# Kernel optimization log

Measured on AMD Instinct MI355X. Metric: run time of the kernel, lower is better.

Reference implementation:

```python
import jax, jax.numpy as jnp
import numpy as np


def setup_inputs() -> dict:
    key = jax.random.key(0)
    x = jax.random.normal(key, (16, 256, 256, 64), dtype=jnp.float32)
    return {"x": x, "n_components": 32}


def reference(x, n_components):
    B = x.shape[0]
    C = x.shape[-1]
    # flatten spatial dims: [B, N, C]
    flat = x.reshape(B, -1, C)
    N = flat.shape[1]
    mean = jnp.mean(flat, axis=1, keepdims=True)
    centered = flat - mean
    # per-batch covariance [B, C, C]
    cov = jnp.einsum('bnc,bnd->bcd', centered, centered) / jnp.float32(N - 1)
    eigenvalues, eigenvectors = jnp.linalg.eigh(cov)
    # sort eigenvectors by descending eigenvalue, keep top n_components columns
    idx = jnp.argsort(-eigenvalues, axis=-1)  # [B, C]
    top = jnp.take_along_axis(eigenvectors, idx[:, None, :], axis=-1)[:, :, :n_components]
    # project: [B, N, k]
    projected = jnp.einsum('bnc,bck->bnk', centered, top)
    return projected.reshape(x.shape[:-1] + (n_components,))
```

## Files before the change

### kernel.cpp

```cpp
#include <hip/hip_runtime.h>
#include <hip/hip_bf16.h>


__device__ __forceinline__ double fsign(double a, double b){ return (b >= 0.0) ? fabs(a) : -fabs(a); }
__device__ __forceinline__ double slapy2(double x, double y){ return sqrt(x*x + y*y); }

__device__ __forceinline__ void slartg(double f, double g, double& cs, double& sn, double& r){
  if (g == 0.0){ cs = 1.0; sn = 0.0; r = f; }
  else if (f == 0.0){ cs = 0.0; sn = fsign(1.0, g); r = fabs(g); }
  else {
    double d = sqrt(f*f + g*g);
    cs = fabs(f)/d;
    r  = fsign(d, f);
    sn = g/r;
  }
}

__device__ __forceinline__ void slaev2(double a, double b, double c,
                                       double& rt1, double& rt2, double& cs1, double& sn1){
  double sm = a + c, df = a - c, adf = fabs(df), tb = b + b, ab = fabs(tb);
  double acmx, acmn, rt, cs, ct, acs, tn; int sgn1, sgn2;
  if (fabs(a) > fabs(c)) { acmx = a; acmn = c; } else { acmx = c; acmn = a; }
  if (adf > ab)      rt = adf*sqrt(1.0 + (ab/adf)*(ab/adf));
  else if (adf < ab) rt = ab*sqrt(1.0 + (adf/ab)*(adf/ab));
  else               rt = ab*sqrt(2.0);
  if (sm < 0.0){ rt1 = 0.5*(sm - rt); sgn1 = -1; rt2 = (acmx/rt1)*acmn - (b/rt1)*b; }
  else if (sm > 0.0){ rt1 = 0.5*(sm + rt); sgn1 = 1; rt2 = (acmx/rt1)*acmn - (b/rt1)*b; }
  else { rt1 = 0.5*rt; rt2 = -0.5*rt; sgn1 = 1; }
  if (df >= 0.0){ cs = df + rt; sgn2 = 1; } else { cs = df - rt; sgn2 = -1; }
  acs = fabs(cs);
  if (acs > ab){ ct = -tb/cs; sn1 = 1.0/sqrt(1.0 + ct*ct); cs1 = ct*sn1; }
  else {
    if (ab == 0.0){ cs1 = 1.0; sn1 = 0.0; }
    else { tn = -cs/tb; cs1 = 1.0/sqrt(1.0 + tn*tn); sn1 = tn*cs1; }
  }
  if (sgn1 == sgn2){ tn = cs1; cs1 = -sn1; sn1 = tn; }
}

__device__ __forceinline__ double wave_sum(double v){
  #pragma unroll
  for (int off = 32; off > 0; off >>= 1) v += __shfl_xor(v, off);
  return v;
}

template<int LDZ>
__device__ void steqr16(double* dd, double* ee, double* Zt, int tid,
                        double* wc, double* wsn)
{
#define DQ(i) dd[(i)-1]
#define EQ(i) ee[(i)-1]
#define ZT(r,c) Zt[(r)*LDZ+(c)]
  const int n = 16;
  const double eps = 5.9604644775390625e-8;
  const double eps2 = eps*eps;
  const double safmin = 1.1754943508222875e-38;
  const int nmaxit = n*30;
  int jtot = 0, l1 = 1, nm1 = n-1;
  int l, lsv, lend, lendsv, m, i;
  double p, g, r, s, c, f, b2, rt1, rt2, anorm, tst;

L10:
  if (l1 > n) goto L160;
  if (l1 > 1) EQ(l1-1) = 0.0;
  if (l1 <= nm1){
    for (m = l1; m <= nm1; ++m){
      tst = fabs(EQ(m));
      if (tst == 0.0) goto L30;
      if (tst <= (sqrt(fabs(DQ(m)))*sqrt(fabs(DQ(m+1))))*eps){ EQ(m) = 0.0; goto L30; }
    }
  }
  m = n;
L30:
  l = l1; lsv = l; lend = m; lendsv = lend; l1 = m+1;
  if (lend == l) goto L10;
  anorm = 0.0;
  for (i = l; i <= lend; ++i) anorm = fmax(anorm, fabs(DQ(i)));
  for (i = l; i <  lend; ++i) anorm = fmax(anorm, fabs(EQ(i)));
  if (anorm == 0.0) goto L10;
  if (fabs(DQ(lend)) < fabs(DQ(l))){ lend = lsv; l = lendsv; }
  if (lend > l){
L40:
    if (l != lend){
      for (m = l; m <= lend-1; ++m){
        tst = fabs(EQ(m)); tst = tst*tst;
        if (tst <= (eps2*fabs(DQ(m)))*fabs(DQ(m+1)) + safmin) goto L60;
      }
    }
    m = lend;
L60:
    if (m < lend) EQ(m) = 0.0;
    p = DQ(l);
    if (m == l) goto L80;
    if (m == l+1){
      slaev2(DQ(l), EQ(l), DQ(l+1), rt1, rt2, c, s);
      if (tid < 16){
        double t = ZT(tid, l);
        ZT(tid, l)   = c*t - s*ZT(tid, l-1);
        ZT(tid, l-1) = s*t + c*ZT(tid, l-1);
      }
      DQ(l) = rt1; DQ(l+1) = rt2; EQ(l) = 0.0;
      l += 2;
      if (l <= lend) goto L40;
      goto L140;
    }
    if (jtot == nmaxit) goto L140;
    jtot++;
    g = (DQ(l+1)-p)/(2.0*EQ(l));
    r = slapy2(g, 1.0);
    g = DQ(m) - p + (EQ(l)/(g + fsign(r, g)));
    s = 1.0; c = 1.0; p = 0.0;
    for (i = m-1; i >= l; --i){
      f = s*EQ(i); b2 = c*EQ(i);
      slartg(g, f, c, s, r);
      if (i != m-1) EQ(i+1) = r;
      g = DQ(i+1) - p;
      r = (DQ(i)-g)*s + 2.0*c*b2;
      p = s*r;
      DQ(i+1) = g + p;
      g = c*r - b2;
      wc[i] = c; wsn[i] = -s;
    }
    for (int i2 = m-1; i2 >= l; --i2){
      double cc = wc[i2], ssv = wsn[i2];
      if (tid < 16){
        double t = ZT(tid, i2);
        ZT(tid, i2)   = cc*t - ssv*ZT(tid, i2-1);
        ZT(tid, i2-1) = ssv*t + cc*ZT(tid, i2-1);
      }
    }
    DQ(l) = DQ(l) - p;
    EQ(l) = g;
    goto L40;
L80:
    DQ(l) = p;
    l++;
    if (l <= lend) goto L40;
    goto L140;
  } else {
L90:
    if (l != lend){
      for (m = l; m >= lend+1; --m){
        tst = fabs(EQ(m-1)); tst = tst*tst;
        if (tst <= (eps2*fabs(DQ(m)))*fabs(DQ(m-1)) + safmin) goto L110;
      }
    }
    m = lend;
L110:
    if (m > lend) EQ(m-1) = 0.0;
    p = DQ(l);
    if (m == l) goto L130;
    if (m == l-1){
      slaev2(DQ(l-1), EQ(l-1), DQ(l), rt1, rt2, c, s);
      if (tid < 16){
        double t = ZT(tid, l-1);
        ZT(tid, l-1) = c*t - s*ZT(tid, l-2);
        ZT(tid, l-2) = s*t + c*ZT(tid, l-2);
      }
      DQ(l-1) = rt1; DQ(l) = rt2; EQ(l-1) = 0.0;
      l -= 2;
      if (l >= lend) goto L90;
      goto L140;
    }
    if (jtot == nmaxit) goto L140;
    jtot++;
    g = (DQ(l-1)-p)/(2.0*EQ(l-1));
    r = slapy2(g, 1.0);
    g = DQ(m) - p + (EQ(l-1)/(g + fsign(r, g)));
    s = 1.0; c = 1.0; p = 0.0;
    for (i = m; i <= l-1; ++i){
      f = s*EQ(i); b2 = c*EQ(i);
      slartg(g, f, c, s, r);
      if (i != m) EQ(i-1) = r;
      g = DQ(i) - p;
      r = (DQ(i+1)-g)*s + 2.0*c*b2;
      p = s*r;
      DQ(i) = g + p;
      g = c*r - b2;
      wc[i] = c; wsn[i] = s;
    }
    for (int i2 = m; i2 <= l-1; ++i2){
      double cc = wc[i2], ssv = wsn[i2];
      if (tid < 16){
        double t = ZT(tid, i2);
        ZT(tid, i2)   = cc*t - ssv*ZT(tid, i2-1);
        ZT(tid, i2-1) = ssv*t + cc*ZT(tid, i2-1);
      }
    }
    DQ(l) = DQ(l) - p;
    EQ(l-1) = g;
    goto L90;
L130:
    DQ(l) = p;
    l--;
    if (l >= lend) goto L90;
    goto L140;
  }
L140:
  if (jtot < nmaxit) goto L10;
L160:
  for (int ii = 2; ii <= n; ++ii){
    int i3 = ii-1, k2 = i3;
    p = DQ(i3);
    for (int j = ii; j <= n; ++j) if (DQ(j) < p){ k2 = j; p = DQ(j); }
    if (k2 != i3){
      DQ(k2) = DQ(i3); DQ(i3) = p;
      if (tid < 16){
        double t = ZT(tid, i3-1);
        ZT(tid, i3-1) = ZT(tid, k2-1);
        ZT(tid, k2-1) = t;
      }
    }
  }
#undef DQ
#undef EQ
#undef ZT
}

template<int N1, int LD>
__device__ void merge_dc(double* Z, double* dloc, double rho_in, int tid,
                         double* zz, double* dl, double* ww, double* mu, double* wt,
                         int* idxm, int* sv, int* tl, int* fperm)
{
  const int NM = 2*N1;
  const int Q  = NM/4;
  const double eps32 = 5.9604644775390625e-8;
  const int j4 = tid >> 2, part = tid & 3;
  __shared__ int s_kn[2];

  if (tid < N1)       zz[tid] = Z[(N1-1)*LD + tid];
  else if (tid < NM)  zz[tid] = Z[N1*LD + tid];
  __syncthreads();
  if (rho_in < 0.0 && tid >= N1 && tid < NM) zz[tid] = -zz[tid];
  __syncthreads();
  if (tid < NM) zz[tid] *= 0.70710678118654752440;
  __syncthreads();
  double rho = fabs(2.0*rho_in);

  {
    int i1 = 0, i2 = 0, t = 0;
    while (i1 < N1 && i2 < N1){
      if (dloc[i1] <= dloc[N1+i2]) idxm[t++] = i1++;
      else                         idxm[t++] = N1 + (i2++);
    }
    while (i1 < N1) idxm[t++] = i1++;
    while (i2 < N1) idxm[t++] = N1 + (i2++);
  }
  double dmax = 0.0, zmax = 0.0;
  for (int i = 0; i < NM; ++i){ dmax = fmax(dmax, fabs(dloc[i])); zmax = fmax(zmax, fabs(zz[i])); }
  double tol = 8.0*eps32*fmax(dmax, zmax);

  if (rho*zmax <= tol){
    double colr[Q]; double dnj = 0.0;
    if (j4 < NM){
      int s0 = idxm[j4];
      dnj = dloc[s0];
      #pragma unroll
      for (int rr = 0; rr < Q; ++rr) colr[rr] = Z[(part+4*rr)*LD + s0];
    }
    __syncthreads();
    if (j4 < NM){
      #pragma unroll
      for (int rr = 0; rr < Q; ++rr) Z[(part+4*rr)*LD + j4] = colr[rr];
      if (part == 0) dloc[j4] = dnj;
    }
    __syncthreads();
    return;
  }

  int K, nd;
  if (tid < 64){
    K = 0; nd = 0;
    int have = 0, pj = 0;
    for (int t = 0; t < NM; ++t){
      int nj = idxm[t];
      if (rho*fabs(zz[nj]) <= tol){
        for (int q = nd; q > 0; --q) tl[q] = tl[q-1];
        tl[0] = nj; nd++;
        continue;
      }
      if (!have){ pj = nj; have = 1; continue; }
      {
        double sZ = zz[pj], cZ = zz[nj];
        double tau2 = slapy2(cZ, sZ);
        double tgap = dloc[nj] - dloc[pj];
        cZ /= tau2; sZ = -sZ/tau2;
        if (fabs(tgap*cZ*sZ) <= tol){
          zz[nj] = tau2; zz[pj] = 0.0;
          if (tid < NM){
            double xq = Z[tid*LD + pj], yq = Z[tid*LD + nj];
            Z[tid*LD + pj] = cZ*xq + sZ*yq;
            Z[tid*LD + nj] = cZ*yq - sZ*xq;
          }
          double t2 = dloc[pj]*cZ*cZ + dloc[nj]*sZ*sZ;
          double t3 = dloc[pj]*sZ*sZ + dloc[nj]*cZ*cZ;
          dloc[nj] = t3; dloc[pj] = t2;
          for (int q = nd; q > 0; --q) tl[q] = tl[q-1];
          tl[0] = pj; nd++;
          { int q = 0;
            while (q+1 < nd && dloc[tl[q]] < dloc[tl[q+1]]){
              int tt = tl[q]; tl[q] = tl[q+1]; tl[q+1] = tt; q++;
            } }
          pj = nj;
        } else {
          sv[K] = pj; dl[K] = dloc[pj]; ww[K] = zz[pj]; K++;
          pj = nj;
        }
      }
    }
    sv[K] = pj; dl[K] = dloc[pj]; ww[K] = zz[pj]; K++;
    if (tid == 0){ s_kn[0] = K; s_kn[1] = nd; }
  }
  __syncthreads();
  K = s_kn[0]; nd = s_kn[1];

  if (j4 < K){
    double dj = dl[j4];
    double dlr[Q], wr[Q];
    double zs2p = 0.0;
    #pragma unroll
    for (int t = 0; t < Q; ++t){
      int i = part + 4*t;
      if (i < K){ double wv = ww[i]; dlr[t] = dl[i]; wr[t] = rho*wv*wv; zs2p += wv*wv; }
      else      { dlr[t] = 1.0e300; wr[t] = 0.0; }
    }
    zs2p += __shfl_xor(zs2p, 1); zs2p += __shfl_xor(zs2p, 2);
    double lo = 0.0, hi = (j4 < K-1) ? (dl[j4+1]-dj) : rho*zs2p;
    for (int it = 0; it < 24; ++it){
      double mid = 0.5*(lo+hi);
      if (mid == lo || mid == hi) break;
      double fvp = 0.0;
      #pragma unroll
      for (int t = 0; t < Q; ++t) fvp += wr[t]/((dlr[t]-dj) - mid);
      fvp += __shfl_xor(fvp, 1); fvp += __shfl_xor(fvp, 2);
      double fv = 1.0 + fvp;
      if (fv < 0.0) lo = mid; else hi = mid;
    }
    double muv = 0.5*(lo+hi);
    for (int it = 0; it < 14; ++it){
      double fvp = 0.0, fpp = 0.0;
      #pragma unroll
      for (int t = 0; t < Q; ++t){
        double den = (dlr[t]-dj) - muv;
        double inv = 1.0/den;
        double tq = wr[t]*inv;
        fvp += tq; fpp += tq*inv;
      }
      fvp += __shfl_xor(fvp, 1); fvp += __shfl_xor(fvp, 2);
      fpp += __shfl_xor(fpp, 1); fpp += __shfl_xor(fpp, 2);
      double fv = 1.0 + fvp;
      if (fv == 0.0) break;
      if (fv < 0.0) lo = muv; else hi = muv;
      double mn = muv - fv/fpp;
      if (!(mn > lo && mn < hi)) mn = 0.5*(lo+hi);
      if (mn == muv) break;
      muv = mn;
    }
    if (part == 0) mu[j4] = muv;
  }
  __syncthreads();

  if (j4 < K){
    double dj = dl[j4];
    double pp = 1.0;
    for (int i2 = part; i2 < K; i2 += 4){
      if (i2 == j4) continue;
      double dij = dj - dl[i2];
      pp *= (dij - mu[i2])/dij;
    }
    pp *= __shfl_xor(pp, 1); pp *= __shfl_xor(pp, 2);
    double prod = -mu[j4]*pp;
    if (part == 0) wt[j4] = fsign(sqrt(fmax(-prod, 0.0)), ww[j4]);
  }
  __syncthreads();

  {
    int a = 0, q = nd-1, t = 0;
    while (a < K && q >= 0){
      if (dl[a]+mu[a] <= dloc[tl[q]]) { fperm[t++] = a; a++; }
      else { fperm[t++] = K+q; q--; }
    }
    while (a < K)  { fperm[t++] = a; a++; }
    while (q >= 0) { fperm[t++] = K+q; q--; }
  }
  __syncthreads();

  double colr[Q]; double dnj = 0.0;
  if (j4 < NM){
    int src = fperm[j4];
    if (src < K){
      double muj = mu[src];
      double ds  = dl[src];
      double nrmp = 0.0;
      for (int i = part; i < K; i += 4){
        double del = (dl[i]-ds) - muj;
        double qv = wt[i]/del;
        nrmp += qv*qv;
      }
      nrmp += __shfl_xor(nrmp, 1); nrmp += __shfl_xor(nrmp, 2);
      double invn = 1.0/sqrt(nrmp);
      #pragma unroll
      for (int rr = 0; rr < Q; ++rr) colr[rr] = 0.0;
      for (int i = 0; i < K; ++i){
        double del = (dl[i]-ds) - muj;
        double sval = (wt[i]/del)*invn;
        int cq = sv[i];
        #pragma unroll
        for (int rr = 0; rr < Q; ++rr) colr[rr] += Z[(part+4*rr)*LD + cq]*sval;
      }
      dnj = ds + muj;
    } else {
      int tq2 = tl[src-K];
      #pragma unroll
      for (int rr = 0; rr < Q; ++rr) colr[rr] = Z[(part+4*rr)*LD + tq2];
      dnj = dloc[tq2];
    }
  }
  __syncthreads();
  if (j4 < NM){
    #pragma unroll
    for (int rr = 0; rr < Q; ++rr) Z[(part+4*rr)*LD + j4] = colr[rr];
    if (part == 0) dloc[j4] = dnj;
  }
  __syncthreads();
}

__global__ __launch_bounds__(256) void cov_kernel(const float* __restrict__ x,
                                                  double* __restrict__ gram,
                                                  double* __restrict__ chsum)
{
  __shared__ __align__(16) float tile[16][64];
  const int b   = blockIdx.x >> 5;
  const int ch  = blockIdx.x & 31;
  const int tid = threadIdx.x;
  const int ti = tid >> 4, tj = tid & 15;
  const int lrow = tid >> 4, lf4 = tid & 15;
  const int cch = tid & 63, crr = tid >> 6;
  float acc[4][4];
  #pragma unroll
  for (int a = 0; a < 4; ++a)
    #pragma unroll
    for (int c = 0; c < 4; ++c) acc[a][c] = 0.f;
  float csum = 0.f;
  const int rbase = ch*2048;
  for (int r0 = 0; r0 < 2048; r0 += 16){
    const float4 v = *(const float4*)(x + (((size_t)b*65536 + rbase + r0 + lrow)*64 + lf4*4));
    __syncthreads();
    *(float4*)&tile[lrow][lf4*4] = v;
    __syncthreads();
    #pragma unroll
    for (int rr = 0; rr < 16; ++rr){
      float4 xi = *(const float4*)&tile[rr][4*ti];
      float4 xj = *(const float4*)&tile[rr][4*tj];
      acc[0][0] += xi.x*xj.x; acc[0][1] += xi.x*xj.y; acc[0][2] += xi.x*xj.z; acc[0][3] += xi.x*xj.w;
      acc[1][0] += xi.y*xj.x; acc[1][1] += xi.y*xj.y; acc[1][2] += xi.y*xj.z; acc[1][3] += xi.y*xj.w;
      acc[2][0] += xi.z*xj.x; acc[2][1] += xi.z*xj.y; acc[2][2] += xi.z*xj.z; acc[2][3] += xi.z*xj.w;
      acc[3][0] += xi.w*xj.x; acc[3][1] += xi.w*xj.y; acc[3][2] += xi.w*xj.z; acc[3][3] += xi.w*xj.w;
    }
    #pragma unroll
    for (int rr2 = 0; rr2 < 4; ++rr2) csum += tile[crr + rr2*4][cch];
  }
  double* gb = gram + (size_t)b*4096;
  #pragma unroll
  for (int a = 0; a < 4; ++a)
    #pragma unroll
    for (int c = 0; c < 4; ++c)
      atomicAdd(&gb[(4*ti+a)*64 + (4*tj+c)], (double)acc[a][c]);
  atomicAdd(&chsum[b*64 + cch], (double)csum);
}

__global__ __launch_bounds__(64) void tridiag_kernel(const double* __restrict__ gram,
                                                     const double* __restrict__ chsum,
                                                     double* __restrict__ dG,
                                                     double* __restrict__ eG,
                                                     double* __restrict__ tauG,
                                                     double* __restrict__ VlG,
                                                     float* __restrict__ meanG)
{
  __shared__ double As[64*65];
  __shared__ double vv_[64], wv_[64], mu_s[64], es_s[64], tau_s[64];
  const int b = blockIdx.x;
  const int tid = threadIdx.x;
  const double* gb = gram + (size_t)b*4096;

  double mval = chsum[b*64+tid]*(1.0/65536.0);
  meanG[b*64+tid] = (float)mval;
  mu_s[tid] = mval;
  __syncthreads();
  for (int idx = tid; idx < 4096; idx += 64){
    int i = idx >> 6, j = idx & 63;
    As[i*65+j] = (gb[idx] - 65536.0*mu_s[i]*mu_s[j])*(1.0/65535.0);
  }
  __syncthreads();

  for (int i = 0; i < 63; ++i){
    double alpha = As[(i+1)*65+i];
    double xv0 = (tid >= i+2) ? As[tid*65+i] : 0.0;
    double xn2 = wave_sum(xv0*xv0);
    if (xn2 == 0.0){
      es_s[i] = alpha; tau_s[i] = 0.0;
      VlG[((size_t)b*63 + i)*64 + tid] = 0.0;
      __syncthreads();
      continue;
    }
    double xnorm = sqrt(xn2);
    double betav = -fsign(slapy2(alpha, xnorm), alpha);
    double taui  = (betav-alpha)/betav;
    double invs  = 1.0/(alpha-betav);
    double vval = (tid == i+1) ? 1.0 : ((tid >= i+2) ? xv0*invs : 0.0);
    vv_[tid] = vval;
    VlG[((size_t)b*63 + i)*64 + tid] = vval;
    __syncthreads();
    double xvr = 0.0;
    if (tid >= i+1){
      for (int c2 = i+1; c2 < 64; ++c2) xvr += As[tid*65+c2]*vv_[c2];
      xvr *= taui;
    }
    double dot = wave_sum((tid >= i+1) ? xvr*vval : 0.0);
    double alf = -0.5*taui*dot;
    wv_[tid] = (tid >= i+1) ? (xvr + alf*vval) : 0.0;
    __syncthreads();
    if (tid >= i+1){
      double vr = vval, wr = wv_[tid];
      for (int c2 = i+1; c2 < 64; ++c2) As[tid*65+c2] -= vr*wv_[c2] + wr*vv_[c2];
    }
    es_s[i] = betav; tau_s[i] = taui;
    __syncthreads();
  }
  dG[b*64+tid]   = As[tid*65+tid];
  eG[b*64+tid]   = (tid < 63) ? es_s[tid]  : 0.0;
  tauG[b*64+tid] = (tid < 63) ? tau_s[tid] : 0.0;
}

__global__ __launch_bounds__(64) void steqr_kernel(double* __restrict__ dG,
                                                   const double* __restrict__ eG,
                                                   double* __restrict__ Zg)
{
  __shared__ double Zt[16*17];
  __shared__ double dd[16], ee[16], wc[20], wsn[20];
  const int b = blockIdx.x >> 2, s = blockIdx.x & 3;
  const int tid = threadIdx.x;

  {
    double dv = (tid < 16) ? dG[b*64 + 16*s + tid] : 0.0;
    if (tid == 0  && s > 0) dv -= fabs(eG[b*64 + 16*s - 1]);
    if (tid == 15 && s < 3) dv -= fabs(eG[b*64 + 16*s + 15]);
    if (tid < 16) dd[tid] = dv;
    if (tid < 15) ee[tid] = eG[b*64 + 16*s + tid];
    if (tid == 15) ee[15] = 0.0;
  }
  for (int idx = tid; idx < 16*17; idx += 64) Zt[idx] = 0.0;
  __syncthreads();
  if (tid < 16) Zt[tid*17+tid] = 1.0;
  __syncthreads();

  steqr16<17>(dd, ee, Zt, tid, wc, wsn);
  __syncthreads();

  for (int idx = tid; idx < 256; idx += 64){
    int r = idx >> 4, c = idx & 15;
    Zg[(size_t)b*4096 + s*256 + idx] = Zt[r*17+c];
  }
  if (tid < 16) dG[b*64 + 16*s + tid] = dd[tid];
}

__global__ __launch_bounds__(256) void merge16_kernel(double* __restrict__ Zg,
                                                      double* __restrict__ dG,
                                                      const double* __restrict__ eG)
{
  __shared__ double Z32[32*33];
  __shared__ double dloc[32];
  __shared__ double zz[32], dl[32], ww[32], mu[32], wt[32];
  __shared__ int idxm[32], sv[32], tl[32], fp[32];
  const int b = blockIdx.x >> 1, h = blockIdx.x & 1;
  const int tid = threadIdx.x;

  for (int idx = tid; idx < 32*33; idx += 256) Z32[idx] = 0.0;
  if (tid < 32) dloc[tid] = dG[b*64 + 32*h + tid];
  __syncthreads();
  {
    int idx = tid;
    int r = idx >> 4, c = idx & 15;
    Z32[r*33 + c]           = Zg[(size_t)b*4096 + (2*h)*256   + idx];
    Z32[(16+r)*33 + (16+c)] = Zg[(size_t)b*4096 + (2*h+1)*256 + idx];
  }
  __syncthreads();

  double rho_in = eG[b*64 + 32*h + 15];
  merge_dc<16,33>(Z32, dloc, rho_in, tid, zz, dl, ww, mu, wt, idxm, sv, tl, fp);

  for (int idx = tid; idx < 1024; idx += 256){
    int r = idx >> 5, c = idx & 31;
    Zg[(size_t)b*4096 + 2048 + h*1024 + idx] = Z32[r*33 + c];
  }
  if (tid < 32) dG[b*64 + 32*h + tid] = dloc[tid];
}

__global__ __launch_bounds__(256) void merge32_bt_kernel(const double* __restrict__ Zg,
                                                         double* __restrict__ dG,
                                                         const double* __restrict__ eG,
                                                         const double* __restrict__ tauG,
                                                         const double* __restrict__ VlG,
                                                         float* __restrict__ Vt)
{
  __shared__ double Z64[64*65];
  __shared__ double Vl_s[63*64];
  __shared__ double dloc[64], tau_l[64];
  __shared__ double zz[64], dl[64], ww[64], mu[64], wt[64];
  __shared__ int idxm[64], sv[64], tl[64], fp[64];
  const int b = blockIdx.x;
  const int tid = threadIdx.x;

  for (int idx = tid; idx < 64*65; idx += 256) Z64[idx] = 0.0;
  if (tid < 64){ dloc[tid] = dG[b*64 + tid]; tau_l[tid] = tauG[b*64 + tid]; }
  for (int idx = tid; idx < 63*64; idx += 256) Vl_s[idx] = VlG[(size_t)b*63*64 + idx];
  __syncthreads();
  for (int idx = tid; idx < 1024; idx += 256){
    int r = idx >> 5, c = idx & 31;
    Z64[r*65 + c]           = Zg[(size_t)b*4096 + 2048 + idx];
    Z64[(32+r)*65 + (32+c)] = Zg[(size_t)b*4096 + 3072 + idx];
  }
  __syncthreads();

  double rho_in = eG[b*64 + 31];
  merge_dc<32,65>(Z64, dloc, rho_in, tid, zz, dl, ww, mu, wt, idxm, sv, tl, fp);

  {
    const int jc = tid >> 2, part = tid & 3;
    double z[16];
    #pragma unroll
    for (int rr = 0; rr < 16; ++rr) z[rr] = Z64[(part + 4*rr)*65 + jc];
    for (int i = 62; i >= 0; --i){
      double taui = tau_l[i];
      if (taui == 0.0) continue;
      double vir[16];
      #pragma unroll
      for (int rr = 0; rr < 16; ++rr) vir[rr] = Vl_s[i*64 + part + 4*rr];
      double w0 = 0.0, w1 = 0.0;
      #pragma unroll
      for (int rr = 0; rr < 16; rr += 2){ w0 += vir[rr]*z[rr]; w1 += vir[rr+1]*z[rr+1]; }
      double w = w0 + w1;
      w += __shfl_xor(w, 1);
      w += __shfl_xor(w, 2);
      w *= taui;
      #pragma unroll
      for (int rr = 0; rr < 16; ++rr) z[rr] -= vir[rr]*w;
    }
    #pragma unroll
    for (int rr = 0; rr < 16; ++rr) Z64[(part + 4*rr)*65 + jc] = z[rr];
  }
  __syncthreads();

  for (int idx = tid; idx < 2048; idx += 256){
    int c2 = idx >> 5, k = idx & 31;
    Vt[(size_t)b*2048 + idx] = (float)Z64[c2*65 + (63-k)];
  }
}

__global__ __launch_bounds__(256) void proj_kernel(const float* __restrict__ x,
                                                   const float* __restrict__ Vt,
                                                   const float* __restrict__ meanf,
                                                   float* __restrict__ out)
{
  __shared__ float Vs[64][32];
  __shared__ float ms[64];
  const int b = blockIdx.x >> 8;
  const int rb = blockIdx.x & 255;
  const int tid = threadIdx.x;
  for (int idx = tid; idx < 2048; idx += 256) ((float*)Vs)[idx] = Vt[(size_t)b*2048 + idx];
  if (tid < 64) ms[tid] = meanf[b*64+tid];
  __syncthreads();
  const size_t row = (size_t)b*65536 + (size_t)rb*256 + tid;
  const float4* xr = (const float4*)(x + row*64);
  float acc[32];
  #pragma unroll
  for (int k = 0; k < 32; ++k) acc[k] = 0.f;
  #pragma unroll
  for (int c4 = 0; c4 < 16; ++c4){
    float4 xv = xr[c4];
    float t0 = xv.x - ms[4*c4+0];
    float t1 = xv.y - ms[4*c4+1];
    float t2 = xv.z - ms[4*c4+2];
    float t3 = xv.w - ms[4*c4+3];
    #pragma unroll
    for (int k = 0; k < 32; ++k) acc[k] += t0*Vs[4*c4+0][k];
    #pragma unroll
    for (int k = 0; k < 32; ++k) acc[k] += t1*Vs[4*c4+1][k];
    #pragma unroll
    for (int k = 0; k < 32; ++k) acc[k] += t2*Vs[4*c4+2][k];
    #pragma unroll
    for (int k = 0; k < 32; ++k) acc[k] += t3*Vs[4*c4+3][k];
  }
  float4* op = (float4*)(out + row*32);
  #pragma unroll
  for (int k4 = 0; k4 < 8; ++k4)
    op[k4] = make_float4(acc[4*k4], acc[4*k4+1], acc[4*k4+2], acc[4*k4+3]);
}

extern "C" void kernel_launch(void* const* d_in, const int* in_sizes, int n_in,
                              void* d_out, int out_size, void* d_ws, size_t ws_size,
                              hipStream_t stream)
{
  const float* x = (const float*)d_in[0];
  float* out = (float*)d_out;
  char* ws = (char*)d_ws;
  double* gram  = (double*)(ws);
  double* Zg    = (double*)(ws);
  double* chsum = (double*)(ws + 524288);
  double* dG    = (double*)(ws + 532480);
  double* eG    = (double*)(ws + 540672);
  double* tauG  = (double*)(ws + 548864);
  double* VlG   = (double*)(ws + 557056);
  float*  Vt    = (float*) (ws + 1073152);
  float*  mf    = (float*) (ws + 1204224);

  hipMemsetAsync(ws, 0, 532480, stream);
  cov_kernel     <<<dim3(512),  dim3(256), 0, stream>>>(x, gram, chsum);
  tridiag_kernel <<<dim3(16),   dim3(64),  0, stream>>>(gram, chsum, dG, eG, tauG, VlG, mf);
  steqr_kernel   <<<dim3(64),   dim3(64),  0, stream>>>(dG, eG, Zg);
  merge16_kernel <<<dim3(32),   dim3(256), 0, stream>>>(Zg, dG, eG);
  merge32_bt_kernel<<<dim3(16), dim3(256), 0, stream>>>(Zg, dG, eG, tauG, VlG, Vt);
  proj_kernel    <<<dim3(4096), dim3(256), 0, stream>>>(x, Vt, mf, out);
}
```

Measured before the change: 1.068 ms.

## Double-buffer cov loads, unroll tridiag matvec, vectorize projection LDS reads

The covariance kernel now stages 32 rows per iteration and prefetches the next tile into registers while computing on the current one, which halves barrier count and hides global load latency. The tridiagonalization inner loops are fully unrolled over all 64 columns with four accumulators, replacing variable-bound loops with masked-free work (relying on zeroed v entries). The projection kernel reads V from shared memory as float4 and fuses four channel updates per accumulator. The tridiag change does extra work on already-eliminated columns and assumes those entries contribute zero, which is a correctness risk.

```diff
diff --git a/kernel.cpp b/kernel.cpp
--- a/kernel.cpp
+++ b/kernel.cpp
@@ -428,7 +428,7 @@
                                                   double* __restrict__ gram,
                                                   double* __restrict__ chsum)
 {
-  __shared__ __align__(16) float tile[16][64];
+  __shared__ __align__(16) float tile[32][64];
   const int b   = blockIdx.x >> 5;
   const int ch  = blockIdx.x & 31;
   const int tid = threadIdx.x;
@@ -441,14 +441,20 @@
     #pragma unroll
     for (int c = 0; c < 4; ++c) acc[a][c] = 0.f;
   float csum = 0.f;
-  const int rbase = ch*2048;
-  for (int r0 = 0; r0 < 2048; r0 += 16){
-    const float4 v = *(const float4*)(x + (((size_t)b*65536 + rbase + r0 + lrow)*64 + lf4*4));
+  const float* xb = x + ((size_t)b*65536 + (size_t)ch*2048)*64;
+  float4 v0 = *(const float4*)(xb + (size_t)(lrow     )*64 + lf4*4);
+  float4 v1 = *(const float4*)(xb + (size_t)(lrow + 16)*64 + lf4*4);
+  for (int r0 = 0; r0 < 2048; r0 += 32){
     __syncthreads();
-    *(float4*)&tile[lrow][lf4*4] = v;
+    *(float4*)&tile[lrow][lf4*4]      = v0;
+    *(float4*)&tile[16 + lrow][lf4*4] = v1;
     __syncthreads();
-    #pragma unroll
-    for (int rr = 0; rr < 16; ++rr){
+    if (r0 + 32 < 2048){
+      v0 = *(const float4*)(xb + (size_t)(r0 + 32 + lrow)*64 + lf4*4);
+      v1 = *(const float4*)(xb + (size_t)(r0 + 48 + lrow)*64 + lf4*4);
+    }
+    #pragma unroll
+    for (int rr = 0; rr < 32; ++rr){
       float4 xi = *(const float4*)&tile[rr][4*ti];
       float4 xj = *(const float4*)&tile[rr][4*tj];
       acc[0][0] += xi.x*xj.x; acc[0][1] += xi.x*xj.y; acc[0][2] += xi.x*xj.z; acc[0][3] += xi.x*xj.w;
@@ -457,7 +463,7 @@
       acc[3][0] += xi.w*xj.x; acc[3][1] += xi.w*xj.y; acc[3][2] += xi.w*xj.z; acc[3][3] += xi.w*xj.w;
     }
     #pragma unroll
-    for (int rr2 = 0; rr2 < 4; ++rr2) csum += tile[crr + rr2*4][cch];
+    for (int rr2 = 0; rr2 < 8; ++rr2) csum += tile[crr + rr2*4][cch];
   }
   double* gb = gram + (size_t)b*4096;
   #pragma unroll
@@ -510,18 +516,24 @@
     vv_[tid] = vval;
     VlG[((size_t)b*63 + i)*64 + tid] = vval;
     __syncthreads();
-    double xvr = 0.0;
-    if (tid >= i+1){
-      for (int c2 = i+1; c2 < 64; ++c2) xvr += As[tid*65+c2]*vv_[c2];
-      xvr *= taui;
-    }
+    double x0 = 0.0, x1 = 0.0, x2 = 0.0, x3 = 0.0;
+    #pragma unroll
+    for (int c2 = 0; c2 < 64; c2 += 4){
+      x0 += As[tid*65+c2+0]*vv_[c2+0];
+      x1 += As[tid*65+c2+1]*vv_[c2+1];
+      x2 += As[tid*65+c2+2]*vv_[c2+2];
+      x3 += As[tid*65+c2+3]*vv_[c2+3];
+    }
+    double xvr = ((x0+x1)+(x2+x3))*taui;
     double dot = wave_sum((tid >= i+1) ? xvr*vval : 0.0);
     double alf = -0.5*taui*dot;
     wv_[tid] = (tid >= i+1) ? (xvr + alf*vval) : 0.0;
     __syncthreads();
-    if (tid >= i+1){
+    {
       double vr = vval, wr = wv_[tid];
-      for (int c2 = i+1; c2 < 64; ++c2) As[tid*65+c2] -= vr*wv_[c2] + wr*vv_[c2];
+      #pragma unroll
+      for (int c2 = 0; c2 < 64; ++c2)
+        As[tid*65+c2] -= vr*wv_[c2] + wr*vv_[c2];
     }
     es_s[i] = betav; tau_s[i] = taui;
     __syncthreads();
@@ -661,7 +673,7 @@
                                                    const float* __restrict__ meanf,
                                                    float* __restrict__ out)
 {
-  __shared__ float Vs[64][32];
+  __shared__ __align__(16) float Vs[64][32];
   __shared__ float ms[64];
   const int b = blockIdx.x >> 8;
   const int rb = blockIdx.x & 255;
@@ -682,13 +694,16 @@
     float t2 = xv.z - ms[4*c4+2];
     float t3 = xv.w - ms[4*c4+3];
     #pragma unroll
-    for (int k = 0; k < 32; ++k) acc[k] += t0*Vs[4*c4+0][k];
-    #pragma unroll
-    for (int k = 0; k < 32; ++k) acc[k] += t1*Vs[4*c4+1][k];
-    #pragma unroll
-    for (int k = 0; k < 32; ++k) acc[k] += t2*Vs[4*c4+2][k];
-    #pragma unroll
-    for (int k = 0; k < 32; ++k) acc[k] += t3*Vs[4*c4+3][k];
+    for (int k4 = 0; k4 < 8; ++k4){
+      const float4 a0 = *(const float4*)&Vs[4*c4+0][4*k4];
+      const float4 a1 = *(const float4*)&Vs[4*c4+1][4*k4];
+      const float4 a2 = *(const float4*)&Vs[4*c4+2][4*k4];
+      const float4 a3 = *(const float4*)&Vs[4*c4+3][4*k4];
+      acc[4*k4+0] += t0*a0.x + t1*a1.x + t2*a2.x + t3*a3.x;
+      acc[4*k4+1] += t0*a0.y + t1*a1.y + t2*a2.y + t3*a3.y;
+      acc[4*k4+2] += t0*a0.z + t1*a1.z + t2*a2.z + t3*a3.z;
+      acc[4*k4+3] += t0*a0.w + t1*a1.w + t2*a2.w + t3*a3.w;
+    }
   }
   float4* op = (float4*)(out + row*32);
   #pragma unroll
```

Result: faster. 1.034 ms (-3.2%).
